# Optimization experiments

Hardware: AMD Instinct MI355X
Metric: run time of the kernel (lower is better)

Reference implementation:

```python
import jax, jax.numpy as jnp
import numpy as np
import math

IN_F = 4096
OUT_F = 4096
NUM_FREQ = 16
RANK = 2
N_TOK = 8192


def setup_inputs() -> dict:
    key = jax.random.key(0)
    ks = jax.random.split(key, 10)
    x = jax.random.normal(ks[0], (N_TOK, IN_F), dtype=jnp.float32)
    amp = jax.random.normal(ks[1], (NUM_FREQ,), dtype=jnp.float32) * 0.1
    rf = jax.random.normal(ks[2], (NUM_FREQ,), dtype=jnp.float32) * 2.0
    cf = jax.random.normal(ks[3], (NUM_FREQ,), dtype=jnp.float32) * 2.0
    rp = jax.random.normal(ks[4], (NUM_FREQ,), dtype=jnp.float32) * 0.5
    cp = jax.random.normal(ks[5], (NUM_FREQ,), dtype=jnp.float32) * 0.5
    lora_A = jax.random.normal(ks[6], (OUT_F, RANK), dtype=jnp.float32) * 0.01
    lora_B = jax.random.normal(ks[7], (RANK, IN_F), dtype=jnp.float32) * 0.01
    alpha = jnp.float32(0.5)
    beta = jnp.float32(0.5)
    bias = jnp.zeros((OUT_F,), dtype=jnp.float32)
    return {"x": x, "amp": amp, "rf": rf, "cf": cf, "rp": rp, "cp": cp,
            "lora_A": lora_A, "lora_B": lora_B, "alpha": alpha, "beta": beta,
            "bias": bias}


def reference(x, amp, rf, cf, rp, cp, lora_A, lora_B, alpha, beta, bias):
    out_f, in_f = lora_A.shape[0], lora_B.shape[1]
    two_pi = 2.0 * math.pi
    r = jnp.linspace(0.0, two_pi, out_f, dtype=jnp.float32)  # [out_f]
    c = jnp.linspace(0.0, two_pi, in_f, dtype=jnp.float32)   # [in_f]
    # Fourier weight synthesis: sum_k amp[k] * outer(sin(r*rf[k]+rp[k]), cos(c*cf[k]+cp[k]))
    S = jnp.sin(r[None, :] * rf[:, None] + rp[:, None])  # [nf, out_f]
    C = jnp.cos(c[None, :] * cf[:, None] + cp[:, None])  # [nf, in_f]
    W_fourier = jnp.einsum('k,ko,ki->oi', amp, S, C)     # [out_f, in_f]
    W_lora = lora_A @ lora_B                              # [out_f, in_f]
    std = math.sqrt(2.0 / (in_f + out_f))
    a = jax.nn.sigmoid(alpha)
    b = jax.nn.sigmoid(beta)
    W = a * jnp.tanh(W_fourier) * std + b * jnp.tanh(W_lora) * std
    return x @ W.T + bias
```

## Files before the change

### kernel.cpp

```cpp
#include <hip/hip_runtime.h>
#include <hip/hip_bf16.h>
#include <cstdint>

typedef __attribute__((ext_vector_type(4))) float f32x4;
typedef __attribute__((ext_vector_type(4))) int i32x4;

#define IN_F 4096
#define OUT_F 4096
#define N_TOK 8192
#define NUM_FREQ 16


__device__ inline float fast_tanh(float x) {
    float ax = fabsf(x);
    float e = __expf(2.0f * ax);
    float t = 1.0f - 2.0f / (e + 1.0f);
    return copysignf(t, x);
}

__device__ inline void load_lds16(const void* g, void* l) {
    __builtin_amdgcn_global_load_lds(
        (const __attribute__((address_space(1))) void*)(uintptr_t)g,
        (__attribute__((address_space(3))) void*)(uint32_t)(uintptr_t)l,
        16, 0, 0);
}

__device__ inline int q8(float v, float s) {
    int q = (int)rintf(v * s);
    return min(127, max(-127, q));
}

__device__ inline unsigned int pack4(int q0, int q1, int q2, int q3) {
    return (q0 & 255) | ((q1 & 255) << 8) | ((q2 & 255) << 16) |
           ((q3 & 255) << 24);
}

__global__ __launch_bounds__(256)
void prep(const float* __restrict__ x, signed char* __restrict__ xq,
          float* __restrict__ sx, const float* __restrict__ amp,
          const float* __restrict__ rf, const float* __restrict__ cf,
          const float* __restrict__ rp, const float* __restrict__ cp,
          const float* __restrict__ lA, const float* __restrict__ lB,
          const float* __restrict__ alpha, const float* __restrict__ beta,
          signed char* __restrict__ wq, float* __restrict__ sw) {
    const int tid = threadIdx.x;
    const int wave = tid >> 6;
    const int lane = tid & 63;
    __shared__ float s_s[NUM_FREQ], s_cf[NUM_FREQ], s_cp[NUM_FREQ];
    __shared__ float red[4];

    if (blockIdx.x < OUT_F) {
        const int o = blockIdx.x;
        const float step = 6.28318530717958647692f / 4095.0f;
        if (tid < NUM_FREQ) {
            float r = step * (float)o;
            s_s[tid] = amp[tid] * __sinf(r * rf[tid] + rp[tid]);
            s_cf[tid] = cf[tid];
            s_cp[tid] = cp[tid];
        }
        __syncthreads();
        const float sa = 1.0f / (1.0f + __expf(-alpha[0]));
        const float sb = 1.0f / (1.0f + __expf(-beta[0]));
        const float stdv = 0.015625f;
        const float a0 = lA[o * 2 + 0];
        const float a1 = lA[o * 2 + 1];

        float w[16];
        const int ibase = tid * 16;
        const f32x4* lB4 = (const f32x4*)lB;
#pragma unroll
        for (int g = 0; g < 4; ++g) {
            f32x4 b0 = lB4[tid * 4 + g];
            f32x4 b1 = lB4[1024 + tid * 4 + g];
#pragma unroll
            for (int e = 0; e < 4; ++e) {
                int j = g * 4 + e;
                float ci = step * (float)(ibase + j);
                float wf = 0.0f;
#pragma unroll
                for (int k = 0; k < NUM_FREQ; ++k)
                    wf += s_s[k] * __cosf(ci * s_cf[k] + s_cp[k]);
                float wl = a0 * b0[e] + a1 * b1[e];
                w[j] = sa * stdv * fast_tanh(wf) + sb * stdv * fast_tanh(wl);
            }
        }
        float m = 0.0f;
#pragma unroll
        for (int j = 0; j < 16; ++j) m = fmaxf(m, fabsf(w[j]));
#pragma unroll
        for (int off = 32; off > 0; off >>= 1)
            m = fmaxf(m, __shfl_xor(m, off));
        if (lane == 0) red[wave] = m;
        __syncthreads();
        m = fmaxf(fmaxf(red[0], red[1]), fmaxf(red[2], red[3]));
        m = fmaxf(m, 1e-20f);
        const float s = 127.0f / m;
        uint4 out;
        unsigned int* op = (unsigned int*)&out;
#pragma unroll
        for (int g = 0; g < 4; ++g)
            op[g] = pack4(q8(w[g * 4], s), q8(w[g * 4 + 1], s),
                          q8(w[g * 4 + 2], s), q8(w[g * 4 + 3], s));
        *(uint4*)(wq + (size_t)o * IN_F + ibase) = out;
        if (tid == 0) sw[o] = m / 127.0f;
    } else {
        const int t = blockIdx.x - OUT_F;
        const f32x4* xr = (const f32x4*)(x + (size_t)t * IN_F);
        f32x4 v[4];
#pragma unroll
        for (int j = 0; j < 4; ++j) v[j] = xr[tid + 256 * j];
        float m = 0.0f;
#pragma unroll
        for (int j = 0; j < 4; ++j)
#pragma unroll
            for (int e = 0; e < 4; ++e) m = fmaxf(m, fabsf(v[j][e]));
#pragma unroll
        for (int off = 32; off > 0; off >>= 1)
            m = fmaxf(m, __shfl_xor(m, off));
        if (lane == 0) red[wave] = m;
        __syncthreads();
        m = fmaxf(fmaxf(red[0], red[1]), fmaxf(red[2], red[3]));
        m = fmaxf(m, 1e-20f);
        const float s = 127.0f / m;
        unsigned int* orow = (unsigned int*)(xq + (size_t)t * IN_F);
#pragma unroll
        for (int j = 0; j < 4; ++j)
            orow[tid + 256 * j] =
                pack4(q8(v[j][0], s), q8(v[j][1], s), q8(v[j][2], s),
                      q8(v[j][3], s));
        if (tid == 0) sx[t] = m / 127.0f;
    }
}

#define BM 256
#define BN 128
#define BKB 128
#define SUBK 64

__global__ __launch_bounds__(256, 2)
void gemm_i8(const signed char* __restrict__ A, const signed char* __restrict__ B,
             const float* __restrict__ sx, const float* __restrict__ sw,
             const float* __restrict__ bias, float* __restrict__ C,
             int M, int N, int K) {
    __shared__ signed char sA[2][BM * SUBK];
    __shared__ signed char sB[2][BN * SUBK];

    const int tid = threadIdx.x;
    const int wave = tid >> 6;
    const int lane = tid & 63;

    const int bm = blockIdx.y * BM;
    const int bn = blockIdx.x * BN;

    const int srow = lane >> 2;
    const int scol = (((lane & 3) ^ ((lane >> 3) & 3)) << 4);

    const signed char* gA = A + (size_t)(bm + wave * 16 + srow) * K + scol;
    const signed char* gB = B + (size_t)(bn + wave * 16 + srow) * K + scol;

    const int lm = lane & 15;
    const int quad = lane >> 4;
    const int kq = ((quad ^ ((lm >> 1) & 3)) << 4);

    const int wm = (wave & 1) * 128;
    const int wn = (wave >> 1) * 64;
    const int aoff = (wm + lm) * SUBK + kq;
    const int boff = (wn + lm) * SUBK + kq;

    i32x4 acc[8][4] = {};

    for (int k0 = 0; k0 < K; k0 += BKB) {
#pragma unroll
        for (int h = 0; h < 2; ++h) {
            const int kk = k0 + h * SUBK;
#pragma unroll
            for (int c = 0; c < 4; ++c)
                load_lds16(gA + (size_t)c * 64 * K + kk,
                           &sA[h][(wave * 16 + c * 64) * SUBK]);
#pragma unroll
            for (int c = 0; c < 2; ++c)
                load_lds16(gB + (size_t)c * 64 * K + kk,
                           &sB[h][(wave * 16 + c * 64) * SUBK]);
        }
        __syncthreads();

#pragma unroll
        for (int h = 0; h < 2; ++h) {
            i32x4 af[8], bv[4];
#pragma unroll
            for (int i = 0; i < 8; ++i)
                af[i] = *(const i32x4*)&sA[h][aoff + i * 16 * SUBK];
#pragma unroll
            for (int i = 0; i < 4; ++i)
                bv[i] = *(const i32x4*)&sB[h][boff + i * 16 * SUBK];

#pragma unroll
            for (int im = 0; im < 8; ++im)
#pragma unroll
                for (int in = 0; in < 4; ++in)
                    acc[im][in] = __builtin_amdgcn_mfma_i32_16x16x64_i8(
                        af[im], bv[in], acc[im][in], 0, 0, 0);
        }

        __syncthreads();
    }

    float sxv[8][4];
#pragma unroll
    for (int im = 0; im < 8; ++im)
#pragma unroll
        for (int r = 0; r < 4; ++r)
            sxv[im][r] = sx[bm + wm + im * 16 + quad * 4 + r];

#pragma unroll
    for (int in = 0; in < 4; ++in) {
        const int cn = bn + wn + in * 16 + lm;
        const float bv_ = bias[cn];
        const float scw = sw[cn];
#pragma unroll
        for (int im = 0; im < 8; ++im) {
            const int rm = bm + wm + im * 16 + quad * 4;
#pragma unroll
            for (int r = 0; r < 4; ++r)
                C[(size_t)(rm + r) * N + cn] =
                    (float)acc[im][in][r] * (sxv[im][r] * scw) + bv_;
        }
    }
}

extern "C" void kernel_launch(void* const* d_in, const int* in_sizes, int n_in,
                              void* d_out, int out_size, void* d_ws,
                              size_t ws_size, hipStream_t stream) {
    const float* x = (const float*)d_in[0];
    const float* amp = (const float*)d_in[1];
    const float* rf = (const float*)d_in[2];
    const float* cf = (const float*)d_in[3];
    const float* rp = (const float*)d_in[4];
    const float* cp = (const float*)d_in[5];
    const float* lA = (const float*)d_in[6];
    const float* lB = (const float*)d_in[7];
    const float* alpha = (const float*)d_in[8];
    const float* beta = (const float*)d_in[9];
    const float* bias = (const float*)d_in[10];
    float* out = (float*)d_out;

    signed char* wq = (signed char*)d_ws;
    signed char* xq = wq + (size_t)OUT_F * IN_F;
    float* sw = (float*)(xq + (size_t)N_TOK * IN_F);
    float* sx = sw + OUT_F;

    prep<<<OUT_F + N_TOK, 256, 0, stream>>>(x, xq, sx, amp, rf, cf, rp, cp,
                                            lA, lB, alpha, beta, wq, sw);
    gemm_i8<<<dim3(OUT_F / BN, N_TOK / BM), 256, 0, stream>>>(
        xq, wq, sx, sw, bias, out, N_TOK, OUT_F, IN_F);
}
```

Before: 452.2 us.

## Compute 4 weight rows per block, sharing cosine evaluations across rows

The weight-synthesis part of the prep kernel now handles four output rows per block. Each group of four lanes splits the 16 frequencies, computes the cosine terms once per column, reuses them for all four rows, and reduces across the group with shuffles. This cuts transcendental work per weight element by about a factor of four. The cost is byte-granular, strided int8 stores instead of 16-byte vector stores, plus extra shuffles and registers.

```diff
diff --git a/kernel.cpp b/kernel.cpp
--- a/kernel.cpp
+++ b/kernel.cpp
@@ -9,6 +9,7 @@
 #define OUT_F 4096
 #define N_TOK 8192
 #define NUM_FREQ 16
+#define RROWS 4
 
 
 __device__ inline float fast_tanh(float x) {
@@ -46,80 +47,136 @@
     const int tid = threadIdx.x;
     const int wave = tid >> 6;
     const int lane = tid & 63;
-    __shared__ float s_s[NUM_FREQ], s_cf[NUM_FREQ], s_cp[NUM_FREQ];
-    __shared__ float red[4];
-
-    if (blockIdx.x < OUT_F) {
-        const int o = blockIdx.x;
+    __shared__ float s_s[RROWS][NUM_FREQ];
+    __shared__ float red[RROWS][4];
+
+    if (blockIdx.x < OUT_F / RROWS) {
+        const int o0 = blockIdx.x * RROWS;
         const float step = 6.28318530717958647692f / 4095.0f;
-        if (tid < NUM_FREQ) {
-            float r = step * (float)o;
-            s_s[tid] = amp[tid] * __sinf(r * rf[tid] + rp[tid]);
-            s_cf[tid] = cf[tid];
-            s_cp[tid] = cp[tid];
-        }
-        __syncthreads();
+        if (tid < RROWS * NUM_FREQ) {
+            const int r = tid >> 4;
+            const int k = tid & 15;
+            s_s[r][k] =
+                amp[k] * __sinf(step * (float)(o0 + r) * rf[k] + rp[k]);
+        }
+        __syncthreads();
+
+        const int g = lane >> 2;
+        const int q = lane & 3;
+
+        float cfr[4], cpr[4];
+#pragma unroll
+        for (int e = 0; e < 4; ++e) {
+            cfr[e] = cf[q * 4 + e];
+            cpr[e] = cp[q * 4 + e];
+        }
+        float skr[RROWS][4];
+#pragma unroll
+        for (int r = 0; r < RROWS; ++r)
+#pragma unroll
+            for (int e = 0; e < 4; ++e) skr[r][e] = s_s[r][q * 4 + e];
+
         const float sa = 1.0f / (1.0f + __expf(-alpha[0]));
         const float sb = 1.0f / (1.0f + __expf(-beta[0]));
         const float stdv = 0.015625f;
-        const float a0 = lA[o * 2 + 0];
-        const float a1 = lA[o * 2 + 1];
-
-        float w[16];
-        const int ibase = tid * 16;
-        const f32x4* lB4 = (const f32x4*)lB;
-#pragma unroll
-        for (int g = 0; g < 4; ++g) {
-            f32x4 b0 = lB4[tid * 4 + g];
-            f32x4 b1 = lB4[1024 + tid * 4 + g];
-#pragma unroll
-            for (int e = 0; e < 4; ++e) {
-                int j = g * 4 + e;
-                float ci = step * (float)(ibase + j);
-                float wf = 0.0f;
-#pragma unroll
-                for (int k = 0; k < NUM_FREQ; ++k)
-                    wf += s_s[k] * __cosf(ci * s_cf[k] + s_cp[k]);
-                float wl = a0 * b0[e] + a1 * b1[e];
-                w[j] = sa * stdv * fast_tanh(wf) + sb * stdv * fast_tanh(wl);
+        float a0r[RROWS], a1r[RROWS];
+#pragma unroll
+        for (int r = 0; r < RROWS; ++r) {
+            a0r[r] = lA[(o0 + r) * 2 + 0];
+            a1r[r] = lA[(o0 + r) * 2 + 1];
+        }
+
+        const int ibw = wave * 1024;
+        float w[RROWS][16];
+
+#pragma unroll
+        for (int j = 0; j < 16; ++j) {
+#pragma unroll
+            for (int sq = 0; sq < 4; ++sq) {
+                const int i = ibw + (j * 4 + sq) * 16 + g;
+                const float ci = step * (float)i;
+                float cv[4];
+#pragma unroll
+                for (int e = 0; e < 4; ++e)
+                    cv[e] = __cosf(ci * cfr[e] + cpr[e]);
+#pragma unroll
+                for (int r = 0; r < RROWS; ++r) {
+                    float p = skr[r][0] * cv[0] + skr[r][1] * cv[1] +
+                              skr[r][2] * cv[2] + skr[r][3] * cv[3];
+                    p += __shfl_xor(p, 1);
+                    p += __shfl_xor(p, 2);
+                    if (q == sq) w[r][j] = p;
+                }
             }
         }
+
+#pragma unroll
+        for (int j = 0; j < 16; ++j) {
+            const int i = ibw + (j * 4 + q) * 16 + g;
+            const float b0 = lB[i];
+            const float b1 = lB[IN_F + i];
+#pragma unroll
+            for (int r = 0; r < RROWS; ++r) {
+                const float wl = a0r[r] * b0 + a1r[r] * b1;
+                w[r][j] = sa * stdv * fast_tanh(w[r][j]) +
+                          sb * stdv * fast_tanh(wl);
+            }
+        }
+
+        float m[RROWS];
+#pragma unroll
+        for (int r = 0; r < RROWS; ++r) {
+            float mm = 0.0f;
+#pragma unroll
+            for (int j = 0; j < 16; ++j) mm = fmaxf(mm, fabsf(w[r][j]));
+#pragma unroll
+            for (int off = 32; off > 0; off >>= 1)
+                mm = fmaxf(mm, __shfl_xor(mm, off));
+            m[r] = mm;
+        }
+        if (lane == 0) {
+#pragma unroll
+            for (int r = 0; r < RROWS; ++r) red[r][wave] = m[r];
+        }
+        __syncthreads();
+#pragma unroll
+        for (int r = 0; r < RROWS; ++r) {
+            float mm = fmaxf(fmaxf(red[r][0], red[r][1]),
+                             fmaxf(red[r][2], red[r][3]));
+            m[r] = fmaxf(mm, 1e-20f);
+        }
+
+#pragma unroll
+        for (int r = 0; r < RROWS; ++r) {
+            const float s = 127.0f / m[r];
+            signed char* wrow = wq + (size_t)(o0 + r) * IN_F;
+#pragma unroll
+            for (int j = 0; j < 16; ++j) {
+                const int i = ibw + (j * 4 + q) * 16 + g;
+                wrow[i] = (signed char)q8(w[r][j], s);
+            }
+        }
+        if (tid == 0) {
+#pragma unroll
+            for (int r = 0; r < RROWS; ++r) sw[o0 + r] = m[r] / 127.0f;
+        }
+    } else {
+        const int t = blockIdx.x - OUT_F / RROWS;
+        const f32x4* xr = (const f32x4*)(x + (size_t)t * IN_F);
+        f32x4 v[4];
+#pragma unroll
+        for (int j = 0; j < 4; ++j) v[j] = xr[tid + 256 * j];
         float m = 0.0f;
 #pragma unroll
-        for (int j = 0; j < 16; ++j) m = fmaxf(m, fabsf(w[j]));
+        for (int j = 0; j < 4; ++j)
+#pragma unroll
+            for (int e = 0; e < 4; ++e) m = fmaxf(m, fabsf(v[j][e]));
 #pragma unroll
         for (int off = 32; off > 0; off >>= 1)
             m = fmaxf(m, __shfl_xor(m, off));
-        if (lane == 0) red[wave] = m;
-        __syncthreads();
-        m = fmaxf(fmaxf(red[0], red[1]), fmaxf(red[2], red[3]));
-        m = fmaxf(m, 1e-20f);
-        const float s = 127.0f / m;
-        uint4 out;
-        unsigned int* op = (unsigned int*)&out;
-#pragma unroll
-        for (int g = 0; g < 4; ++g)
-            op[g] = pack4(q8(w[g * 4], s), q8(w[g * 4 + 1], s),
-                          q8(w[g * 4 + 2], s), q8(w[g * 4 + 3], s));
-        *(uint4*)(wq + (size_t)o * IN_F + ibase) = out;
-        if (tid == 0) sw[o] = m / 127.0f;
-    } else {
-        const int t = blockIdx.x - OUT_F;
-        const f32x4* xr = (const f32x4*)(x + (size_t)t * IN_F);
-        f32x4 v[4];
-#pragma unroll
-        for (int j = 0; j < 4; ++j) v[j] = xr[tid + 256 * j];
-        float m = 0.0f;
-#pragma unroll
-        for (int j = 0; j < 4; ++j)
-#pragma unroll
-            for (int e = 0; e < 4; ++e) m = fmaxf(m, fabsf(v[j][e]));
-#pragma unroll
-        for (int off = 32; off > 0; off >>= 1)
-            m = fmaxf(m, __shfl_xor(m, off));
-        if (lane == 0) red[wave] = m;
-        __syncthreads();
-        m = fmaxf(fmaxf(red[0], red[1]), fmaxf(red[2], red[3]));
+        if (lane == 0) red[0][wave] = m;
+        __syncthreads();
+        m = fmaxf(fmaxf(red[0][0], red[0][1]), fmaxf(red[0][2], red[0][3]));
         m = fmaxf(m, 1e-20f);
         const float s = 127.0f / m;
         unsigned int* orow = (unsigned int*)(xq + (size_t)t * IN_F);
@@ -249,8 +306,8 @@
     float* sw = (float*)(xq + (size_t)N_TOK * IN_F);
     float* sx = sw + OUT_F;
 
-    prep<<<OUT_F + N_TOK, 256, 0, stream>>>(x, xq, sx, amp, rf, cf, rp, cp,
-                                            lA, lB, alpha, beta, wq, sw);
+    prep<<<OUT_F / RROWS + N_TOK, 256, 0, stream>>>(
+        x, xq, sx, amp, rf, cf, rp, cp, lA, lB, alpha, beta, wq, sw);
     gemm_i8<<<dim3(OUT_F / BN, N_TOK / BM), 256, 0, stream>>>(
         xq, wq, sx, sw, bias, out, N_TOK, OUT_F, IN_F);
 }
```

Result: faster. 430.0 us (-4.9%).
